# Performance work log

Hardware: AMD Instinct MI355X
Metric: run time of the kernel (lower is better)

## Reference

```python
import jax, jax.numpy as jnp
import numpy as np

VOCAB = 32000
ROUTE_BIAS = 10.0  # weight on the deterministic one-hot route vs mu logits


def setup_inputs() -> dict:
    key = jax.random.key(0)
    k1, k2, k3, k4, k5, k6 = jax.random.split(key, 6)
    B, S, H = 2, 4096, 1024
    E, Ie = 8, 512  # intermediate_size=4096 -> expert_intermediate=512, fused dim=2*Ie=1024
    return {
        "hidden_states": jax.random.normal(k1, (B, S, H), dtype=jnp.float32),
        "token_ids": jax.random.randint(k2, (B, S), 0, VOCAB),
        "mu": jax.random.normal(k3, (B, S, H), dtype=jnp.float32),
        "gate_up_proj": jax.random.normal(k4, (E, H, 2 * Ie), dtype=jnp.float32) * 0.02,
        "down_proj": jax.random.normal(k5, (E, Ie, H), dtype=jnp.float32) * 0.02,
        "mu_router_w": jax.random.normal(k6, (E, H), dtype=jnp.float32) * 0.02,
    }


def reference(hidden_states, token_ids, mu, gate_up_proj, down_proj, mu_router_w):
    B, S, H = hidden_states.shape
    E, _, F2 = gate_up_proj.shape
    Ie = F2 // 2
    N = B * S

    # deterministic token->expert routing, optionally perturbed by mu logits
    token_to_expert = jnp.arange(VOCAB, dtype=jnp.int32) % E
    base_expert = token_to_expert[jnp.clip(token_ids, 0, VOCAB - 1)]      # [B,S]
    mu_logits = jnp.einsum('bsh,eh->bse', mu, mu_router_w)                 # [B,S,E]
    combined = jax.nn.one_hot(base_expert, E, dtype=mu_logits.dtype) * ROUTE_BIAS + mu_logits
    expert_ids = jnp.argmax(combined, axis=-1).reshape(N)                  # [N]

    x = hidden_states.reshape(N, H)
    tok = jnp.arange(N)

    # compute per-expert GEMM then select per-token expert output
    # (same math as gathering the full weight slab per token, without the
    #  N*H*2Ie gathered-weight blowup of the original torch code)
    gu_all = jnp.einsum('nh,ehf->enf', x, gate_up_proj)                    # [E,N,2Ie]
    gu = gu_all[expert_ids, tok]                                           # [N,2Ie]
    gate, up = gu[:, :Ie], gu[:, Ie:]
    inter = jax.nn.silu(gate) * up                                         # [N,Ie]

    z_all = jnp.einsum('ni,eih->enh', inter, down_proj)                    # [E,N,H]
    out = z_all[expert_ids, tok].reshape(B, S, H)
    return out
```

## Files before the change

### kernel.cpp

```cpp
#include <hip/hip_runtime.h>
#include <hip/hip_bf16.h>
#include <stdint.h>

typedef __bf16 bf16x8 __attribute__((ext_vector_type(8)));
typedef float f32x4 __attribute__((ext_vector_type(4)));

#define ROUTE_BIAS_F 10.0f
#define VOCAB_SZ 32000

__device__ __forceinline__ unsigned short f2bf(float f) {
    union { float f; unsigned u; } v; v.f = f;
    unsigned u = v.u;
    unsigned r = u + 0x7FFFu + ((u >> 16) & 1u);
    return (unsigned short)(r >> 16);
}
__device__ __forceinline__ float bf2f(unsigned short s) {
    union { unsigned u; float f; } v; v.u = ((unsigned)s) << 16;
    return v.f;
}
__device__ __forceinline__ void ld16(const unsigned short* g, unsigned short* l) {
    __builtin_amdgcn_global_load_lds(
        (const __attribute__((address_space(1))) void*)g,
        (__attribute__((address_space(3))) void*)l, 16, 0, 0);
}

__global__ void k_prep(const float* __restrict__ hidden, const float* __restrict__ mu,
                       const int* __restrict__ tok_ids, const float* __restrict__ rw,
                       unsigned short* __restrict__ xb, int* __restrict__ eids,
                       int H, int N) {
    int lane = threadIdx.x & 63;
    int wv   = threadIdx.x >> 6;
    int tok  = blockIdx.x * 4 + wv;
    if (tok >= N) return;
    const float4* hp = (const float4*)(hidden + (size_t)tok * H);
    const float4* mp = (const float4*)(mu + (size_t)tok * H);
    const float4* rp = (const float4*)rw;
    ushort4* xp = (ushort4*)(xb + (size_t)tok * H);
    int H4 = H >> 2;
    float acc[8];
#pragma unroll
    for (int e = 0; e < 8; ++e) acc[e] = 0.f;
#pragma unroll
    for (int j = 0; j < 4; ++j) {
        int idx = lane + 64 * j;
        float4 h4 = hp[idx];
        ushort4 o;
        o.x = f2bf(h4.x); o.y = f2bf(h4.y); o.z = f2bf(h4.z); o.w = f2bf(h4.w);
        xp[idx] = o;
        float4 m4 = mp[idx];
#pragma unroll
        for (int e = 0; e < 8; ++e) {
            float4 w4 = rp[e * H4 + idx];
            acc[e] += m4.x * w4.x + m4.y * w4.y + m4.z * w4.z + m4.w * w4.w;
        }
    }
#pragma unroll
    for (int e = 0; e < 8; ++e) {
        float v = acc[e];
#pragma unroll
        for (int off = 32; off > 0; off >>= 1) v += __shfl_xor(v, off);
        acc[e] = v;
    }
    if (lane == 0) {
        int t = tok_ids[tok];
        if (t < 0) t = 0;
        if (t > VOCAB_SZ - 1) t = VOCAB_SZ - 1;
        int be = t % 8;
        float best = -1e30f; int bi = 0;
#pragma unroll
        for (int e = 0; e < 8; ++e) {
            float v = acc[e] + (e == be ? ROUTE_BIAS_F : 0.f);
            if (v > best) { best = v; bi = e; }
        }
        eids[tok] = bi;
    }
}

__global__ void k_transpose_all(const float* __restrict__ gup, const float* __restrict__ dnp,
                                unsigned short* __restrict__ wgut, unsigned short* __restrict__ wdnt,
                                int H, int F2, int Ie) {
    __shared__ float tile[32][33];
    int z = blockIdx.z;
    const float* inp; unsigned short* outp; int R, C;
    if (z < 8) { R = H; C = F2; inp = gup + (size_t)z * R * C;       outp = wgut + (size_t)z * R * C; }
    else       { R = Ie; C = H; inp = dnp + (size_t)(z - 8) * R * C; outp = wdnt + (size_t)(z - 8) * R * C; }
    int c0 = blockIdx.x * 32, r0 = blockIdx.y * 32;
    if (r0 >= R || c0 >= C) return;
    int tx = threadIdx.x, ty = threadIdx.y;
#pragma unroll
    for (int k = 0; k < 32; k += 8)
        tile[ty + k][tx] = inp[(size_t)(r0 + ty + k) * C + c0 + tx];
    __syncthreads();
#pragma unroll
    for (int k = 0; k < 32; k += 8)
        outp[(size_t)(c0 + ty + k) * R + r0 + tx] = f2bf(tile[tx][ty + k]);
}

__global__ void k_count(const int* __restrict__ eids,
                        int* __restrict__ blockcnt, int N) {
    __shared__ int cnt[8];
    int tid = threadIdx.x;
    if (tid < 8) cnt[tid] = 0;
    __syncthreads();
    int tok = blockIdx.x * 256 + tid;
    int lane = tid & 63;
    int eid = (tok < N) ? eids[tok] : -1;
#pragma unroll
    for (int e = 0; e < 8; ++e) {
        unsigned long long m = __ballot(eid == e);
        if (lane == 0 && m) atomicAdd(&cnt[e], __popcll(m));
    }
    __syncthreads();
    if (tid < 8) blockcnt[blockIdx.x * 8 + tid] = cnt[tid];
}

__global__ void k_scan(const int* __restrict__ blockcnt,
                       int* __restrict__ counts, int* __restrict__ base_,
                       int* __restrict__ offs, int NB) {
    __shared__ int tot[8];
    int lane = threadIdx.x;
    int e = lane >> 3, g = lane & 7;
    int v[4];
    int s = 0;
#pragma unroll
    for (int i = 0; i < 4; ++i) { v[i] = s; s += blockcnt[(g * 4 + i) * 8 + e]; }
    int inc = s;
#pragma unroll
    for (int d = 1; d < 8; d <<= 1) {
        int t = __shfl_up(inc, d);
        if (g >= d) inc += t;
    }
    int excl = inc - s;
#pragma unroll
    for (int i = 0; i < 4; ++i) offs[(g * 4 + i) * 8 + e] = excl + v[i];
    if (g == 7) { counts[e] = inc; tot[e] = inc; }
    __syncthreads();
    if (lane == 0) {
        int s2 = 0;
#pragma unroll
        for (int i = 0; i < 8; ++i) { base_[i] = s2; s2 += tot[i]; }
    }
}

__global__ void k_scatter(const int* __restrict__ eids,
                          const int* __restrict__ offs,
                          int* __restrict__ list, int N) {
    __shared__ int wavecnt[4][8];
    int tid = threadIdx.x;
    int lane = tid & 63, wv = tid >> 6;
    int tok = blockIdx.x * 256 + tid;
    int eid = (tok < N) ? eids[tok] : -1;
    unsigned long long below = (1ull << lane) - 1ull;
    int myrank = 0;
#pragma unroll
    for (int e = 0; e < 8; ++e) {
        unsigned long long m = __ballot(eid == e);
        if (lane == 0) wavecnt[wv][e] = __popcll(m);
        if (eid == e) myrank = __popcll(m & below);
    }
    __syncthreads();
    if (eid >= 0) {
        int pre = 0;
        for (int w = 0; w < wv; ++w) pre += wavecnt[w][eid];
        int pos = offs[blockIdx.x * 8 + eid] + pre + myrank;
        list[eid * N + pos] = tok;
    }
}

#define TM 64
#define TN 128
#define TK 64

__global__ __launch_bounds__(128, 3) void k_gemm_gateup(
    const unsigned short* __restrict__ X,
    const unsigned short* __restrict__ Wt,
    unsigned short* __restrict__ IT,
    const int* __restrict__ counts, const int* __restrict__ base_,
    const int* __restrict__ list, int N, int H, int Ie) {
    int bid = blockIdx.x;
    int e = bid & 7;
    int t = bid >> 3;
    int nt = t & 7;
    int mt = t >> 3;
    int cnt = counts[e];
    int m0 = mt * TM;
    if (m0 >= cnt) return;
    int F2 = 2 * Ie;

    __shared__ __align__(16) unsigned short As[TM * TK];
    __shared__ __align__(16) unsigned short Bs[TN * TK];

    int tid = threadIdx.x;
    int lane = tid & 63, wv = tid >> 6;
    int wn = wv * 64;

    int rowg = lane >> 3;
    int sl   = (lane & 7) ^ rowg;

    const unsigned short* ag[4];
    const unsigned short* bg[8];
#pragma unroll
    for (int i = 0; i < 4; ++i) {
        int r = wv * 32 + i * 8 + rowg;
        int gr = m0 + r;
        int tokrow = (gr < cnt) ? list[e * N + gr] : 0;
        ag[i] = X + (size_t)tokrow * H + sl * 8;
    }
#pragma unroll
    for (int i = 0; i < 8; ++i) {
        int r = wv * 64 + i * 8 + rowg;
        int wrow = (r & 1) * Ie + nt * 64 + (r >> 1);
        bg[i] = Wt + ((size_t)e * F2 + wrow) * H + sl * 8;
    }

    f32x4 acc[4][4];
#pragma unroll
    for (int i = 0; i < 4; ++i)
#pragma unroll
        for (int j = 0; j < 4; ++j) acc[i][j] = (f32x4)(0.f);

    int q = lane >> 4, m = lane & 15;
    int sw = m & 7;

    for (int k0 = 0; k0 < H; k0 += TK) {
#pragma unroll
        for (int i = 0; i < 4; ++i)
            ld16(ag[i] + k0, &As[(wv * 32 + i * 8) * TK]);
#pragma unroll
        for (int i = 0; i < 8; ++i)
            ld16(bg[i] + k0, &Bs[(wv * 64 + i * 8) * TK]);
        __syncthreads();
#pragma unroll
        for (int ks = 0; ks < TK; ks += 32) {
            int kc = ks >> 3;
            int ck = ((kc + q) ^ sw) << 3;
            bf16x8 af[4], bfr[4];
#pragma unroll
            for (int im = 0; im < 4; ++im)
                af[im] = *(const bf16x8*)&As[(m + im * 16) * TK + ck];
#pragma unroll
            for (int in_ = 0; in_ < 4; ++in_)
                bfr[in_] = *(const bf16x8*)&Bs[(wn + m + in_ * 16) * TK + ck];
#pragma unroll
            for (int im = 0; im < 4; ++im)
#pragma unroll
                for (int in_ = 0; in_ < 4; ++in_)
                    acc[im][in_] = __builtin_amdgcn_mfma_f32_16x16x32_bf16(
                        af[im], bfr[in_], acc[im][in_], 0, 0, 0);
        }
        __syncthreads();
    }

    int b = base_[e];
    int nt64 = nt * 64;
#pragma unroll
    for (int im = 0; im < 4; ++im) {
#pragma unroll
        for (int j = 0; j < 4; ++j) {
            int row = im * 16 + q * 4 + j;
            int gr = m0 + row;
#pragma unroll
            for (int in_ = 0; in_ < 4; ++in_) {
                float v = acc[im][in_][j];
                float u = __shfl_xor(v, 1);
                float g = v;
                float s = g / (1.f + __expf(-g));
                float res = s * u;
                if (!(lane & 1) && gr < cnt) {
                    int oc = nt64 + ((wn + in_ * 16 + m) >> 1);
                    IT[(size_t)(b + gr) * Ie + oc] = f2bf(res);
                }
            }
        }
    }
}

__global__ __launch_bounds__(128, 3) void k_gemm_down(
    const unsigned short* __restrict__ IT,
    const unsigned short* __restrict__ Wt,
    float* __restrict__ OUT,
    const int* __restrict__ counts, const int* __restrict__ base_,
    const int* __restrict__ list, int N, int Ie, int H) {
    int bid = blockIdx.x;
    int e = bid & 7;
    int t = bid >> 3;
    int nt = t & 7;
    int mt = t >> 3;
    int cnt = counts[e];
    int m0 = mt * TM;
    if (m0 >= cnt) return;
    int n0 = nt * TN;
    int b = base_[e];

    __shared__ __align__(16) unsigned short As[TM * TK];
    __shared__ __align__(16) unsigned short Bs[TN * TK];

    int tid = threadIdx.x;
    int lane = tid & 63, wv = tid >> 6;
    int wn = wv * 64;

    int rowg = lane >> 3;
    int sl   = (lane & 7) ^ rowg;

    const unsigned short* We = Wt + ((size_t)e * H + n0) * Ie;
    const unsigned short* ag[4];
    const unsigned short* bg[8];
#pragma unroll
    for (int i = 0; i < 4; ++i) {
        int r = wv * 32 + i * 8 + rowg;
        int gr = m0 + r;
        int arow = (gr < cnt) ? (b + gr) : b;
        ag[i] = IT + (size_t)arow * Ie + sl * 8;
    }
#pragma unroll
    for (int i = 0; i < 8; ++i) {
        int r = wv * 64 + i * 8 + rowg;
        bg[i] = We + (size_t)r * Ie + sl * 8;
    }

    f32x4 acc[4][4];
#pragma unroll
    for (int i = 0; i < 4; ++i)
#pragma unroll
        for (int j = 0; j < 4; ++j) acc[i][j] = (f32x4)(0.f);

    int q = lane >> 4, m = lane & 15;
    int sw = m & 7;

    for (int k0 = 0; k0 < Ie; k0 += TK) {
#pragma unroll
        for (int i = 0; i < 4; ++i)
            ld16(ag[i] + k0, &As[(wv * 32 + i * 8) * TK]);
#pragma unroll
        for (int i = 0; i < 8; ++i)
            ld16(bg[i] + k0, &Bs[(wv * 64 + i * 8) * TK]);
        __syncthreads();
#pragma unroll
        for (int ks = 0; ks < TK; ks += 32) {
            int kc = ks >> 3;
            int ck = ((kc + q) ^ sw) << 3;
            bf16x8 af[4], bfr[4];
#pragma unroll
            for (int im = 0; im < 4; ++im)
                af[im] = *(const bf16x8*)&As[(m + im * 16) * TK + ck];
#pragma unroll
            for (int in_ = 0; in_ < 4; ++in_)
                bfr[in_] = *(const bf16x8*)&Bs[(wn + m + in_ * 16) * TK + ck];
#pragma unroll
            for (int im = 0; im < 4; ++im)
#pragma unroll
                for (int in_ = 0; in_ < 4; ++in_)
                    acc[im][in_] = __builtin_amdgcn_mfma_f32_16x16x32_bf16(
                        af[im], bfr[in_], acc[im][in_], 0, 0, 0);
        }
        __syncthreads();
    }

#pragma unroll
    for (int im = 0; im < 4; ++im) {
#pragma unroll
        for (int j = 0; j < 4; ++j) {
            int row = im * 16 + q * 4 + j;
            int gr = m0 + row;
            if (gr < cnt) {
                int tok = list[e * N + gr];
                float* orow = OUT + (size_t)tok * H + n0;
#pragma unroll
                for (int in_ = 0; in_ < 4; ++in_) {
                    int col = wn + in_ * 16 + m;
                    orow[col] = acc[im][in_][j];
                }
            }
        }
    }
}

extern "C" void kernel_launch(void* const* d_in, const int* in_sizes, int n_in,
                              void* d_out, int out_size, void* d_ws, size_t ws_size,
                              hipStream_t stream) {
    const float* hidden   = (const float*)d_in[0];
    const int*   tok_ids  = (const int*)d_in[1];
    const float* mu       = (const float*)d_in[2];
    const float* gup      = (const float*)d_in[3];
    const float* dnp      = (const float*)d_in[4];
    const float* rw       = (const float*)d_in[5];
    float* out = (float*)d_out;

    int N  = in_sizes[1];
    int H  = in_sizes[0] / N;
    int E  = in_sizes[5] / H;
    int F2 = in_sizes[3] / (E * H);
    int Ie = F2 / 2;

    int NB = (N + 255) / 256;

    char* ws = (char*)d_ws;
    size_t o = 0;
    auto alloc = [&](size_t sz) {
        size_t r = o;
        o += (sz + 255) & ~(size_t)255;
        return r;
    };
    int* counts   = (int*)(ws + alloc((size_t)E * 4));
    int* base_    = (int*)(ws + alloc((size_t)E * 4));
    int* eids     = (int*)(ws + alloc((size_t)N * 4));
    int* blockcnt = (int*)(ws + alloc((size_t)NB * 8 * 4));
    int* offs     = (int*)(ws + alloc((size_t)NB * 8 * 4));
    int* list     = (int*)(ws + alloc((size_t)E * N * 4));
    unsigned short* xb   = (unsigned short*)(ws + alloc((size_t)N * H * 2));
    unsigned short* wgut = (unsigned short*)(ws + alloc((size_t)E * F2 * H * 2));
    unsigned short* wdnt = (unsigned short*)(ws + alloc((size_t)E * H * Ie * 2));
    unsigned short* it   = (unsigned short*)(ws + alloc((size_t)N * Ie * 2));

    k_prep<<<dim3((N + 3) / 4), dim3(256), 0, stream>>>(hidden, mu, tok_ids, rw, xb, eids, H, N);

    k_transpose_all<<<dim3(32, 32, 16), dim3(32, 8), 0, stream>>>(gup, dnp, wgut, wdnt, H, F2, Ie);

    k_count<<<dim3(NB), dim3(256), 0, stream>>>(eids, blockcnt, N);
    k_scan<<<dim3(1), dim3(64), 0, stream>>>(blockcnt, counts, base_, offs, NB);
    k_scatter<<<dim3(NB), dim3(256), 0, stream>>>(eids, offs, list, N);

    int MT = (N + TM - 1) / TM;
    k_gemm_gateup<<<dim3(E * MT * (Ie / 64)), dim3(128), 0, stream>>>(
        xb, wgut, it, counts, base_, list, N, H, Ie);

    k_gemm_down<<<dim3(E * MT * (H / TN)), dim3(128), 0, stream>>>(
        it, wdnt, out, counts, base_, list, N, Ie, H);
}
```

Baseline: 225.3 us.

## Enlarge GEMM tiles to 128x128 with 4 waves and vectorize weight transpose

Both expert GEMMs move from a 64x128 tile on 2 waves to a 128x128 tile on 4 waves arranged 2x2. Each wave still computes a 64x64 sub-tile, but B-tile loads are now shared across twice as many rows, which cuts global and LDS traffic for the weights. The weight transpose kernel now uses 64x64 tiles with float4 loads and ushort4 stores to improve memory efficiency. The trade-off is fewer blocks, more padding waste on the last partial M tile per expert, and more LDS per block, which may lower occupancy.

```diff
diff --git a/kernel.cpp b/kernel.cpp
--- a/kernel.cpp
+++ b/kernel.cpp
@@ -76,24 +76,39 @@
     }
 }
 
-__global__ void k_transpose_all(const float* __restrict__ gup, const float* __restrict__ dnp,
-                                unsigned short* __restrict__ wgut, unsigned short* __restrict__ wdnt,
-                                int H, int F2, int Ie) {
-    __shared__ float tile[32][33];
+__global__ __launch_bounds__(256) void k_transpose_all(
+        const float* __restrict__ gup, const float* __restrict__ dnp,
+        unsigned short* __restrict__ wgut, unsigned short* __restrict__ wdnt,
+        int H, int F2, int Ie) {
+    __shared__ float tile[64][65];
     int z = blockIdx.z;
     const float* inp; unsigned short* outp; int R, C;
     if (z < 8) { R = H; C = F2; inp = gup + (size_t)z * R * C;       outp = wgut + (size_t)z * R * C; }
     else       { R = Ie; C = H; inp = dnp + (size_t)(z - 8) * R * C; outp = wdnt + (size_t)(z - 8) * R * C; }
-    int c0 = blockIdx.x * 32, r0 = blockIdx.y * 32;
-    if (r0 >= R || c0 >= C) return;
-    int tx = threadIdx.x, ty = threadIdx.y;
-#pragma unroll
-    for (int k = 0; k < 32; k += 8)
-        tile[ty + k][tx] = inp[(size_t)(r0 + ty + k) * C + c0 + tx];
+    int c0 = blockIdx.x * 64, r0 = blockIdx.y * 64;
+    if (r0 >= R) return;
+    int tid = threadIdx.x;
+    int tr = tid >> 4;
+    int tc = (tid & 15) * 4;
+#pragma unroll
+    for (int p = 0; p < 4; ++p) {
+        float4 v = *(const float4*)&inp[(size_t)(r0 + tr + 16 * p) * C + c0 + tc];
+        tile[tr + 16 * p][tc + 0] = v.x;
+        tile[tr + 16 * p][tc + 1] = v.y;
+        tile[tr + 16 * p][tc + 2] = v.z;
+        tile[tr + 16 * p][tc + 3] = v.w;
+    }
     __syncthreads();
 #pragma unroll
-    for (int k = 0; k < 32; k += 8)
-        outp[(size_t)(c0 + ty + k) * R + r0 + tx] = f2bf(tile[tx][ty + k]);
+    for (int p = 0; p < 4; ++p) {
+        int c = tr + 16 * p;
+        ushort4 o;
+        o.x = f2bf(tile[tc + 0][c]);
+        o.y = f2bf(tile[tc + 1][c]);
+        o.z = f2bf(tile[tc + 2][c]);
+        o.w = f2bf(tile[tc + 3][c]);
+        *(ushort4*)&outp[(size_t)(c0 + c) * R + r0 + tc] = o;
+    }
 }
 
 __global__ void k_count(const int* __restrict__ eids,
@@ -167,11 +182,11 @@
     }
 }
 
-#define TM 64
+#define TM 128
 #define TN 128
 #define TK 64
 
-__global__ __launch_bounds__(128, 3) void k_gemm_gateup(
+__global__ __launch_bounds__(256, 3) void k_gemm_gateup(
     const unsigned short* __restrict__ X,
     const unsigned short* __restrict__ Wt,
     unsigned short* __restrict__ IT,
@@ -192,13 +207,14 @@
 
     int tid = threadIdx.x;
     int lane = tid & 63, wv = tid >> 6;
-    int wn = wv * 64;
+    int wr = (wv >> 1) * 64;
+    int wc = (wv & 1) * 64;
 
     int rowg = lane >> 3;
     int sl   = (lane & 7) ^ rowg;
 
     const unsigned short* ag[4];
-    const unsigned short* bg[8];
+    const unsigned short* bg[4];
 #pragma unroll
     for (int i = 0; i < 4; ++i) {
         int r = wv * 32 + i * 8 + rowg;
@@ -207,8 +223,8 @@
         ag[i] = X + (size_t)tokrow * H + sl * 8;
     }
 #pragma unroll
-    for (int i = 0; i < 8; ++i) {
-        int r = wv * 64 + i * 8 + rowg;
+    for (int i = 0; i < 4; ++i) {
+        int r = wv * 32 + i * 8 + rowg;
         int wrow = (r & 1) * Ie + nt * 64 + (r >> 1);
         bg[i] = Wt + ((size_t)e * F2 + wrow) * H + sl * 8;
     }
@@ -227,8 +243,8 @@
         for (int i = 0; i < 4; ++i)
             ld16(ag[i] + k0, &As[(wv * 32 + i * 8) * TK]);
 #pragma unroll
-        for (int i = 0; i < 8; ++i)
-            ld16(bg[i] + k0, &Bs[(wv * 64 + i * 8) * TK]);
+        for (int i = 0; i < 4; ++i)
+            ld16(bg[i] + k0, &Bs[(wv * 32 + i * 8) * TK]);
         __syncthreads();
 #pragma unroll
         for (int ks = 0; ks < TK; ks += 32) {
@@ -237,10 +253,10 @@
             bf16x8 af[4], bfr[4];
 #pragma unroll
             for (int im = 0; im < 4; ++im)
-                af[im] = *(const bf16x8*)&As[(m + im * 16) * TK + ck];
+                af[im] = *(const bf16x8*)&As[(wr + m + im * 16) * TK + ck];
 #pragma unroll
             for (int in_ = 0; in_ < 4; ++in_)
-                bfr[in_] = *(const bf16x8*)&Bs[(wn + m + in_ * 16) * TK + ck];
+                bfr[in_] = *(const bf16x8*)&Bs[(wc + m + in_ * 16) * TK + ck];
 #pragma unroll
             for (int im = 0; im < 4; ++im)
 #pragma unroll
@@ -257,7 +273,7 @@
     for (int im = 0; im < 4; ++im) {
 #pragma unroll
         for (int j = 0; j < 4; ++j) {
-            int row = im * 16 + q * 4 + j;
+            int row = wr + im * 16 + q * 4 + j;
             int gr = m0 + row;
 #pragma unroll
             for (int in_ = 0; in_ < 4; ++in_) {
@@ -267,7 +283,7 @@
                 float s = g / (1.f + __expf(-g));
                 float res = s * u;
                 if (!(lane & 1) && gr < cnt) {
-                    int oc = nt64 + ((wn + in_ * 16 + m) >> 1);
+                    int oc = nt64 + ((wc + in_ * 16 + m) >> 1);
                     IT[(size_t)(b + gr) * Ie + oc] = f2bf(res);
                 }
             }
@@ -275,7 +291,7 @@
     }
 }
 
-__global__ __launch_bounds__(128, 3) void k_gemm_down(
+__global__ __launch_bounds__(256, 3) void k_gemm_down(
     const unsigned short* __restrict__ IT,
     const unsigned short* __restrict__ Wt,
     float* __restrict__ OUT,
@@ -297,14 +313,15 @@
 
     int tid = threadIdx.x;
     int lane = tid & 63, wv = tid >> 6;
-    int wn = wv * 64;
+    int wr = (wv >> 1) * 64;
+    int wc = (wv & 1) * 64;
 
     int rowg = lane >> 3;
     int sl   = (lane & 7) ^ rowg;
 
     const unsigned short* We = Wt + ((size_t)e * H + n0) * Ie;
     const unsigned short* ag[4];
-    const unsigned short* bg[8];
+    const unsigned short* bg[4];
 #pragma unroll
     for (int i = 0; i < 4; ++i) {
         int r = wv * 32 + i * 8 + rowg;
@@ -313,8 +330,8 @@
         ag[i] = IT + (size_t)arow * Ie + sl * 8;
     }
 #pragma unroll
-    for (int i = 0; i < 8; ++i) {
-        int r = wv * 64 + i * 8 + rowg;
+    for (int i = 0; i < 4; ++i) {
+        int r = wv * 32 + i * 8 + rowg;
         bg[i] = We + (size_t)r * Ie + sl * 8;
     }
 
@@ -332,8 +349,8 @@
         for (int i = 0; i < 4; ++i)
             ld16(ag[i] + k0, &As[(wv * 32 + i * 8) * TK]);
 #pragma unroll
-        for (int i = 0; i < 8; ++i)
-            ld16(bg[i] + k0, &Bs[(wv * 64 + i * 8) * TK]);
+        for (int i = 0; i < 4; ++i)
+            ld16(bg[i] + k0, &Bs[(wv * 32 + i * 8) * TK]);
         __syncthreads();
 #pragma unroll
         for (int ks = 0; ks < TK; ks += 32) {
@@ -342,10 +359,10 @@
             bf16x8 af[4], bfr[4];
 #pragma unroll
             for (int im = 0; im < 4; ++im)
-                af[im] = *(const bf16x8*)&As[(m + im * 16) * TK + ck];
+                af[im] = *(const bf16x8*)&As[(wr + m + im * 16) * TK + ck];
 #pragma unroll
             for (int in_ = 0; in_ < 4; ++in_)
-                bfr[in_] = *(const bf16x8*)&Bs[(wn + m + in_ * 16) * TK + ck];
+                bfr[in_] = *(const bf16x8*)&Bs[(wc + m + in_ * 16) * TK + ck];
 #pragma unroll
             for (int im = 0; im < 4; ++im)
 #pragma unroll
@@ -360,14 +377,14 @@
     for (int im = 0; im < 4; ++im) {
 #pragma unroll
         for (int j = 0; j < 4; ++j) {
-            int row = im * 16 + q * 4 + j;
+            int row = wr + im * 16 + q * 4 + j;
             int gr = m0 + row;
             if (gr < cnt) {
                 int tok = list[e * N + gr];
                 float* orow = OUT + (size_t)tok * H + n0;
 #pragma unroll
                 for (int in_ = 0; in_ < 4; ++in_) {
-                    int col = wn + in_ * 16 + m;
+                    int col = wc + in_ * 16 + m;
                     orow[col] = acc[im][in_][j];
                 }
             }
@@ -414,16 +431,16 @@
 
     k_prep<<<dim3((N + 3) / 4), dim3(256), 0, stream>>>(hidden, mu, tok_ids, rw, xb, eids, H, N);
 
-    k_transpose_all<<<dim3(32, 32, 16), dim3(32, 8), 0, stream>>>(gup, dnp, wgut, wdnt, H, F2, Ie);
+    k_transpose_all<<<dim3(16, 16, 16), dim3(256), 0, stream>>>(gup, dnp, wgut, wdnt, H, F2, Ie);
 
     k_count<<<dim3(NB), dim3(256), 0, stream>>>(eids, blockcnt, N);
     k_scan<<<dim3(1), dim3(64), 0, stream>>>(blockcnt, counts, base_, offs, NB);
     k_scatter<<<dim3(NB), dim3(256), 0, stream>>>(eids, offs, list, N);
 
     int MT = (N + TM - 1) / TM;
-    k_gemm_gateup<<<dim3(E * MT * (Ie / 64)), dim3(128), 0, stream>>>(
+    k_gemm_gateup<<<dim3(E * MT * (Ie / 64)), dim3(256), 0, stream>>>(
         xb, wgut, it, counts, base_, list, N, H, Ie);
 
-    k_gemm_down<<<dim3(E * MT * (H / TN)), dim3(128), 0, stream>>>(
+    k_gemm_down<<<dim3(E * MT * (H / TN)), dim3(256), 0, stream>>>(
         it, wdnt, out, counts, base_, list, N, Ie, H);
 }
```

Measured after the change: 219.0 us. 1.03x faster.
